# Kernel tuning notes

Measured on AMD Instinct MI355X. Metric: run time of the kernel, lower is better.

Reference implementation:

```python
import jax, jax.numpy as jnp
import numpy as np

DROPOUT = 0.2  # dropout radius in normalized [0,1] coords
EPS = 1e-08


def setup_inputs() -> dict:
    key = jax.random.key(0)
    k1, k2, k3, k4 = jax.random.split(key, 4)
    B, C, T = 64, 273, 3000
    brain_sig = jax.random.normal(k1, (B, C, T), dtype=jnp.float32)
    positions = jax.random.uniform(k2, (B, C, 2), dtype=jnp.float32)
    center = jax.random.uniform(k3, (2,), dtype=jnp.float32)
    mc_centers = jax.random.uniform(k4, (100, 2), dtype=jnp.float32)
    return {"brain_sig": brain_sig, "positions": positions,
            "center": center, "mc_centers": mc_centers}


def reference(brain_sig, positions, center, mc_centers):
    # kept channels: distance from ban center > dropout radius  -> (B, C)
    kept = jnp.linalg.norm(positions - center, axis=-1) > DROPOUT
    out = brain_sig * kept[:, :, None].astype(brain_sig.dtype)
    # Monte-Carlo estimate of keep probability (100 trials, vectorized)
    # diffs: (N, B, C, 2)
    diffs = positions[None, :, :, :] - mc_centers[:, None, None, :]
    kept_mc = jnp.linalg.norm(diffs, axis=-1) > DROPOUT  # (N, B, C)
    proba_kept = jnp.mean(kept_mc.astype(brain_sig.dtype), axis=0)  # (B, C)
    out = out / (EPS + proba_kept[:, :, None])
    return out
```

## Files before the change

### kernel.cpp

```cpp
#include <hip/hip_runtime.h>
#include <math.h>


typedef float v4f __attribute__((ext_vector_type(4)));

__global__ __launch_bounds__(256) void channel_dropout_kernel(
    const float* __restrict__ sig,
    const float* __restrict__ pos,
    const float* __restrict__ center,
    const float* __restrict__ mc,
    float* __restrict__ out,
    int T, int NMC)
{
    const int row  = blockIdx.x;
    const int t    = threadIdx.x;
    const int lane = t & 63;

    const size_t base = (size_t)row * (size_t)T;
    const int n4 = T >> 2;
    const v4f* __restrict__ in4  = (const v4f*)(sig + base);
    v4f* __restrict__       out4 = (v4f*)(out + base);

    v4f v[4];
    #pragma unroll
    for (int u = 0; u < 4; ++u) {
        const int i = t + u * 256;
        if (i < n4) v[u] = __builtin_nontemporal_load(in4 + i);
    }

    const float px = pos[2 * row + 0];
    const float py = pos[2 * row + 1];
    const float cx = center[0];
    const float cy = center[1];

    float cnt = 0.0f;
    for (int i = lane; i < NMC; i += 64) {
        const float dx = px - mc[2 * i + 0];
        const float dy = py - mc[2 * i + 1];
        cnt += (sqrtf(dx * dx + dy * dy) > 0.2f) ? 1.0f : 0.0f;
    }
    #pragma unroll
    for (int off = 32; off > 0; off >>= 1)
        cnt += __shfl_xor(cnt, off, 64);

    const float ddx  = px - cx;
    const float ddy  = py - cy;
    const float kept = (sqrtf(ddx * ddx + ddy * ddy) > 0.2f) ? 1.0f : 0.0f;
    const float scale = kept / (1e-8f + cnt / (float)NMC);

    #pragma unroll
    for (int u = 0; u < 4; ++u) {
        const int i = t + u * 256;
        if (i < n4) {
            v4f r = v[u];
            r *= scale;
            __builtin_nontemporal_store(r, out4 + i);
        }
    }
    for (int i = t + 1024; i < n4; i += 256) {
        v4f r = __builtin_nontemporal_load(in4 + i);
        r *= scale;
        __builtin_nontemporal_store(r, out4 + i);
    }
    for (int i = (n4 << 2) + t; i < T; i += 256) {
        out[base + i] = sig[base + i] * scale;
    }
}

extern "C" void kernel_launch(void* const* d_in, const int* in_sizes, int n_in,
                              void* d_out, int out_size, void* d_ws, size_t ws_size,
                              hipStream_t stream) {
    const float* sig    = (const float*)d_in[0];
    const float* pos    = (const float*)d_in[1];
    const float* center = (const float*)d_in[2];
    const float* mc     = (const float*)d_in[3];
    float* out          = (float*)d_out;

    const int rows = in_sizes[1] / 2;
    const int T    = in_sizes[0] / rows;
    const int NMC  = in_sizes[3] / 2;

    channel_dropout_kernel<<<rows, 256, 0, stream>>>(
        sig, pos, center, mc, out, T, NMC);
}
```

Measured before the change: 341.1 us.

## Split per-row scale computation into separate kernel before streaming multiply

Adds a small kernel that computes each row's keep/probability scale with one thread per row, using Monte-Carlo centers staged in shared memory, and writes the scales to the workspace. A second streaming kernel then reads that scale and performs the vectorized load-scale-store, with a smaller register prefetch depth of 3 instead of 4. The aim is to remove the per-block Monte-Carlo loop and wave reduction from the bandwidth-bound streaming path. The cost is an extra launch, a dependency between the two kernels and a workspace round trip. The old fused kernel stays as a fallback.

```diff
diff --git a/kernel.cpp b/kernel.cpp
--- a/kernel.cpp
+++ b/kernel.cpp
@@ -3,8 +3,77 @@
 
 
 typedef float v4f __attribute__((ext_vector_type(4)));
+typedef float v2f __attribute__((ext_vector_type(2)));
 
-__global__ __launch_bounds__(256) void channel_dropout_kernel(
+__global__ __launch_bounds__(256) void scale_kernel(
+    const float* __restrict__ pos,
+    const float* __restrict__ center,
+    const float* __restrict__ mc,
+    float* __restrict__ scale,
+    int rows, int NMC)
+{
+    __shared__ float s_mc[256];
+    const int t = threadIdx.x;
+    for (int i = t; i < 2 * NMC; i += 256) s_mc[i] = mc[i];
+    __syncthreads();
+
+    const int row = blockIdx.x * 256 + t;
+    if (row >= rows) return;
+
+    const v2f p = *(const v2f*)(pos + 2 * (size_t)row);
+    float cnt = 0.0f;
+    for (int i = 0; i < NMC; ++i) {
+        const float dx = p.x - s_mc[2 * i + 0];
+        const float dy = p.y - s_mc[2 * i + 1];
+        cnt += (sqrtf(dx * dx + dy * dy) > 0.2f) ? 1.0f : 0.0f;
+    }
+    const float ddx  = p.x - center[0];
+    const float ddy  = p.y - center[1];
+    const float kept = (sqrtf(ddx * ddx + ddy * ddy) > 0.2f) ? 1.0f : 0.0f;
+    scale[row] = kept / (1e-8f + cnt / (float)NMC);
+}
+
+__global__ __launch_bounds__(256) void stream_kernel(
+    const float* __restrict__ sig,
+    const float* __restrict__ scale_arr,
+    float* __restrict__ out,
+    int T)
+{
+    const int row = blockIdx.x;
+    const float scale = scale_arr[row];
+    const int t = threadIdx.x;
+
+    const size_t base = (size_t)row * (size_t)T;
+    const int n4 = T >> 2;
+    const v4f* __restrict__ in4  = (const v4f*)(sig + base);
+    v4f* __restrict__       out4 = (v4f*)(out + base);
+
+    v4f v[3];
+    #pragma unroll
+    for (int u = 0; u < 3; ++u) {
+        const int i = t + u * 256;
+        if (i < n4) v[u] = __builtin_nontemporal_load(in4 + i);
+    }
+    #pragma unroll
+    for (int u = 0; u < 3; ++u) {
+        const int i = t + u * 256;
+        if (i < n4) {
+            v4f r = v[u];
+            r *= scale;
+            __builtin_nontemporal_store(r, out4 + i);
+        }
+    }
+    for (int i = t + 768; i < n4; i += 256) {
+        v4f r = __builtin_nontemporal_load(in4 + i);
+        r *= scale;
+        __builtin_nontemporal_store(r, out4 + i);
+    }
+    for (int i = (n4 << 2) + t; i < T; i += 256) {
+        out[base + i] = sig[base + i] * scale;
+    }
+}
+
+__global__ __launch_bounds__(256) void fused_kernel(
     const float* __restrict__ sig,
     const float* __restrict__ pos,
     const float* __restrict__ center,
@@ -30,9 +99,6 @@
 
     const float px = pos[2 * row + 0];
     const float py = pos[2 * row + 1];
-    const float cx = center[0];
-    const float cy = center[1];
-
     float cnt = 0.0f;
     for (int i = lane; i < NMC; i += 64) {
         const float dx = px - mc[2 * i + 0];
@@ -43,8 +109,8 @@
     for (int off = 32; off > 0; off >>= 1)
         cnt += __shfl_xor(cnt, off, 64);
 
-    const float ddx  = px - cx;
-    const float ddy  = py - cy;
+    const float ddx  = px - center[0];
+    const float ddy  = py - center[1];
     const float kept = (sqrtf(ddx * ddx + ddy * ddy) > 0.2f) ? 1.0f : 0.0f;
     const float scale = kept / (1e-8f + cnt / (float)NMC);
 
@@ -80,6 +146,15 @@
     const int T    = in_sizes[0] / rows;
     const int NMC  = in_sizes[3] / 2;
 
-    channel_dropout_kernel<<<rows, 256, 0, stream>>>(
-        sig, pos, center, mc, out, T, NMC);
+    if (d_ws != nullptr && ws_size >= (size_t)rows * sizeof(float)
+        && NMC <= 128) {
+        float* scale = (float*)d_ws;
+        const int sblocks = (rows + 255) / 256;
+        scale_kernel<<<sblocks, 256, 0, stream>>>(
+            pos, center, mc, scale, rows, NMC);
+        stream_kernel<<<rows, 256, 0, stream>>>(sig, scale, out, T);
+    } else {
+        fused_kernel<<<rows, 256, 0, stream>>>(
+            sig, pos, center, mc, out, T, NMC);
+    }
 }
```

New measurement: 350.2 us. 1.03x slower.
